# Kernel tuning notes

Hardware: AMD Instinct MI355X
Metric: run time of the kernel (lower is better)

## Reference

```python
import jax, jax.numpy as jnp
import numpy as np

# Per-task block sizes, sorted descending (powers of 2), as in _InverseLogDetCache
N = (262144, 65536, 16384)
TOTAL = 262144 + 65536 + 16384  # 344064
DIAG_SHIFT = 10.0  # keeps Schur complement S away from 0 (plays role of noise)


def setup_inputs() -> dict:
    key = jax.random.key(0)
    ks = jax.random.split(key, 14)
    rn = lambda k, n: jax.random.normal(k, (n,), dtype=jnp.float32)
    return {
        "lam00_re": rn(ks[0], N[0]) + DIAG_SHIFT,
        "lam00_im": rn(ks[1], N[0]),
        "lam01_re": rn(ks[2], N[0]),
        "lam01_im": rn(ks[3], N[0]),
        "lam02_re": rn(ks[4], N[0]),
        "lam02_im": rn(ks[5], N[0]),
        "lam11_re": rn(ks[6], N[1]) + DIAG_SHIFT,
        "lam11_im": rn(ks[7], N[1]),
        "lam12_re": rn(ks[8], N[1]),
        "lam12_im": rn(ks[9], N[1]),
        "lam22_re": rn(ks[10], N[2]) + DIAG_SHIFT,
        "lam22_im": rn(ks[11], N[2]),
        "z_re": rn(ks[12], TOTAL),
        "z_im": rn(ks[13], TOTAL),
    }


def _step(A, B, lam_ll, n_l):
    """One recursive block Schur-complement update.
    A: (Ra, Ra, na) complex current inverse; B: (Ra*r, n_l) off-diag lam block;
    lam_ll: (n_l,) diagonal lam; returns updated A (R+1, R+1, n_l) and logdet inc."""
    Ra, na = A.shape[0], A.shape[-1]
    r = na // n_l
    Bvec = B.reshape(Ra, -1)                              # (Ra, na)
    T = (Bvec[None, :, :] * A).sum(1).reshape(-1, n_l)    # (R, n_l), R = Ra*r
    M = (B.conj() * T).sum(0)                             # (n_l,)
    S = lam_ll - M                                        # Schur complement diag
    logdet_inc = jnp.log(jnp.abs(S)).sum()
    P = T / S                                             # (R, n_l)
    C = P[:, None, :] * T[None, :, :].conj()              # (R, R, n_l)
    # scatter-add old inverse A into the refined block structure of C
    ii0, ii1, ii2 = jnp.meshgrid(jnp.arange(Ra), jnp.arange(Ra), jnp.arange(na), indexing='ij')
    ii0, ii1, ii2 = ii0.ravel(), ii1.ravel(), ii2.ravel()
    jj0 = ii2 % n_l
    jj1 = ii2 // n_l
    C = C.at[ii0 * r + jj1, ii1 * r + jj1, jj0].add(A.reshape(-1))
    ur = jnp.concatenate([C, -P[:, None, :]], axis=1)                       # (R, R+1, n_l)
    br = jnp.concatenate([-P.conj()[None, :, :], (1.0 / S)[None, None, :]], axis=1)  # (1, R+1, n_l)
    return jnp.concatenate([ur, br], axis=0), logdet_inc


def _forward(lams, z):
    A = (1.0 / lams[(0, 0)])[None, None, :]               # (1, 1, N[0])
    logdet = jnp.log(jnp.abs(lams[(0, 0)])).sum()
    for l in range(1, len(N)):
        B = jnp.concatenate([lams[(k, l)] for k in range(l)], axis=0).reshape(-1, N[l])
        A, inc = _step(A, B, lams[(l, l)], N[l])
        logdet = logdet + inc
    # tilde-to-tilde gram matrix solve: z (TOTAL,) -> (1, R, n_min) * A, sum block rows
    n_min = N[-1]
    zb = z.reshape(1, -1, n_min)                          # (1, 21, n_min)
    zout = (zb * A).sum(-2).reshape(-1)                   # (TOTAL,)
    return A, logdet, zout


def reference(lam00_re, lam00_im, lam01_re, lam01_im, lam02_re, lam02_im,
              lam11_re, lam11_im, lam12_re, lam12_im, lam22_re, lam22_im,
              z_re, z_im):
    lams = {
        (0, 0): lam00_re + 1j * lam00_im,
        (0, 1): lam01_re + 1j * lam01_im,
        (0, 2): lam02_re + 1j * lam02_im,
        (1, 1): lam11_re + 1j * lam11_im,
        (1, 2): lam12_re + 1j * lam12_im,
        (2, 2): lam22_re + 1j * lam22_im,
    }
    z = z_re + 1j * z_im
    A, logdet, zout = _forward(lams, z)
    return (jnp.stack([A.real, A.imag]), logdet, jnp.stack([zout.real, zout.imag]))
```

## Files before the change

### kernel.cpp

```cpp
#include <hip/hip_runtime.h>

#define N2 16384
#define N1 65536

#define OUT_AIM 7225344
#define OUT_LD  14450688
#define OUT_ZRE 14450689
#define OUT_ZIM 14794753

#define L_T2R  0
#define L_T2I  1280
#define L_M2   2560
#define L_SC   3072
#define L_IS2R 9728
#define L_IS2I 9792
#define L_RED  9856
#define L_TOT  9864

#define SC(idx, u, jl) lds[L_SC + (((idx)*4 + (u)) * 64) + (jl)]

__global__ __launch_bounds__(448) void fused_kernel(
    const float* __restrict__ l00r, const float* __restrict__ l00i,
    const float* __restrict__ l01r, const float* __restrict__ l01i,
    const float* __restrict__ l02r, const float* __restrict__ l02i,
    const float* __restrict__ l11r, const float* __restrict__ l11i,
    const float* __restrict__ l12r, const float* __restrict__ l12i,
    const float* __restrict__ l22r, const float* __restrict__ l22i,
    const float* __restrict__ zre,  const float* __restrict__ zim,
    float* __restrict__ out, double* __restrict__ ld_partial)
{
    __shared__ float lds[L_TOT];
    const int t   = threadIdx.x;
    const int jl  = t & 63;
    const int j0  = blockIdx.x * 64;
    const bool y0 = (blockIdx.y == 0);
    float ld = 0.f;

    if (t < 256) {
        const int u = t >> 6;
        const int m = u * N2 + (j0 + jl);

        float i0r[4], i0i[4], t1r[4], t1i[4], p1r[4], p1i[4];
        float m1r = 0.f, m1i = 0.f;
#pragma unroll
        for (int k = 0; k < 4; ++k) {
            const int i = k * N1 + m;
            const float ar = l00r[i], ai = l00i[i];
            const float br = l01r[i], bi = l01i[i];
            const float d  = ar*ar + ai*ai;
            const float rd = 1.f / d;
            if (y0) ld += 0.5f * logf(d);
            const float xr = ar * rd, xi = -ai * rd;
            i0r[k] = xr; i0i[k] = xi;
            const float tr = br*xr - bi*xi;
            const float ti = br*xi + bi*xr;
            t1r[k] = tr; t1i[k] = ti;
            m1r += br*tr + bi*ti;
            m1i += br*ti - bi*tr;
        }
        const float s1r = l11r[m] - m1r;
        const float s1i = l11i[m] - m1i;
        const float ds1 = s1r*s1r + s1i*s1i;
        if (y0) ld += 0.5f * logf(ds1);
        const float rds1 = 1.f / ds1;
        const float is1r = s1r * rds1, is1i = -s1i * rds1;
#pragma unroll
        for (int k = 0; k < 4; ++k) {
            p1r[k] = t1r[k]*is1r - t1i[k]*is1i;
            p1i[k] = t1r[k]*is1i + t1i[k]*is1r;
        }

        float bcr[5], bci[5];
#pragma unroll
        for (int a = 0; a < 4; ++a) { bcr[a] = l02r[a*N1+m]; bci[a] = l02i[a*N1+m]; }
        bcr[4] = l12r[m]; bci[4] = l12i[m];

        float wr = -bcr[4], wi = -bci[4];
#pragma unroll
        for (int b = 0; b < 4; ++b) {
            wr += bcr[b]*t1r[b] + bci[b]*t1i[b];
            wi += bci[b]*t1r[b] - bcr[b]*t1i[b];
        }
        float ur[5], ui[5];
#pragma unroll
        for (int a = 0; a < 4; ++a) {
            ur[a] = p1r[a]*wr - p1i[a]*wi + bcr[a]*i0r[a] - bci[a]*i0i[a];
            ui[a] = p1r[a]*wi + p1i[a]*wr + bcr[a]*i0i[a] + bci[a]*i0r[a];
        }
        {
            float vr = bcr[4]*is1r - bci[4]*is1i;
            float vi = bcr[4]*is1i + bci[4]*is1r;
#pragma unroll
            for (int b = 0; b < 4; ++b) {
                vr -= bcr[b]*p1r[b] + bci[b]*p1i[b];
                vi -= bci[b]*p1r[b] - bcr[b]*p1i[b];
            }
            ur[4] = vr; ui[4] = vi;
        }
        float m2r = 0.f, m2i = 0.f;
#pragma unroll
        for (int a = 0; a < 5; ++a) {
            lds[L_T2R + (a*4+u)*64 + jl] = ur[a];
            lds[L_T2I + (a*4+u)*64 + jl] = ui[a];
            m2r += bcr[a]*ur[a] + bci[a]*ui[a];
            m2i += bcr[a]*ui[a] - bci[a]*ur[a];
        }
        lds[L_M2 + (0*4+u)*64 + jl] = m2r;
        lds[L_M2 + (1*4+u)*64 + jl] = m2i;
#pragma unroll
        for (int b = 0; b < 4; ++b) {
            SC(b,      u, jl) = t1r[b];  SC(4+b,  u, jl) = t1i[b];
            SC(8+b,    u, jl) = p1r[b];  SC(12+b, u, jl) = p1i[b];
            SC(16+b,   u, jl) = i0r[b];  SC(20+b, u, jl) = i0i[b];
        }
        SC(24, u, jl) = is1r;  SC(25, u, jl) = is1i;
    }
    __syncthreads();

    if (t < 64) {
        float s2r = l22r[j0 + t], s2i = l22i[j0 + t];
#pragma unroll
        for (int u = 0; u < 4; ++u) {
            s2r -= lds[L_M2 + (0*4+u)*64 + t];
            s2i -= lds[L_M2 + (1*4+u)*64 + t];
        }
        const float ds2  = s2r*s2r + s2i*s2i;
        const float rds2 = 1.f / ds2;
        lds[L_IS2R + t] =  s2r * rds2;
        lds[L_IS2I + t] = -s2i * rds2;
        if (y0) ld += 0.5f * logf(ds2);
    }
    __syncthreads();

    const int g = t >> 6;
    const int p = blockIdx.y * 7 + g;
    const int j = j0 + jl;
    const float is2r = lds[L_IS2R + jl];
    const float is2i = lds[L_IS2I + jl];

    float zr[21], zi[21];
#pragma unroll
    for (int q = 0; q < 21; ++q) { zr[q] = zre[q*N2+j]; zi[q] = zim[q*N2+j]; }

    float zar = 0.f, zai = 0.f;
    if (p == 20) {
#pragma unroll
        for (int q = 0; q < 21; ++q) {
            float ar, ai;
            if (q < 20) {
                const float tqr = lds[L_T2R + q*64 + jl];
                const float tqi = lds[L_T2I + q*64 + jl];
                ar = -(tqr*is2r - tqi*is2i);
                ai =  (tqr*is2i + tqi*is2r);
            } else { ar = is2r; ai = is2i; }
            out[(p*21 + q)*N2 + j]           = ar;
            out[OUT_AIM + (p*21 + q)*N2 + j] = ai;
            zar += zr[q]*ar - zi[q]*ai;
            zai += zr[q]*ai + zi[q]*ar;
        }
    } else {
        const int a_p = p >> 2, u_p = p & 3;
        const float tpr = lds[L_T2R + p*64 + jl];
        const float tpi = lds[L_T2I + p*64 + jl];
        const float ppr = tpr*is2r - tpi*is2i;
        const float ppi = tpr*is2i + tpi*is2r;
        float sar[5], sai[5];
        if (a_p < 4) {
            const float par = SC(8+a_p, u_p, jl), pai = SC(12+a_p, u_p, jl);
#pragma unroll
            for (int b = 0; b < 4; ++b) {
                const float tbr = SC(b, u_p, jl), tbi = SC(4+b, u_p, jl);
                sar[b] = par*tbr + pai*tbi;
                sai[b] = pai*tbr - par*tbi;
            }
            sar[a_p] += SC(16+a_p, u_p, jl);
            sai[a_p] += SC(20+a_p, u_p, jl);
            sar[4] = -par; sai[4] = -pai;
        } else {
#pragma unroll
            for (int b = 0; b < 4; ++b) {
                sar[b] = -SC(8+b,  u_p, jl);
                sai[b] =  SC(12+b, u_p, jl);
            }
            sar[4] = SC(24, u_p, jl);
            sai[4] = SC(25, u_p, jl);
        }
#pragma unroll
        for (int q = 0; q < 21; ++q) {
            float ar, ai;
            if (q < 20) {
                const float tqr = lds[L_T2R + q*64 + jl];
                const float tqi = lds[L_T2I + q*64 + jl];
                ar = ppr*tqr + ppi*tqi;
                ai = ppi*tqr - ppr*tqi;
                if ((q & 3) == u_p) { ar += sar[q>>2]; ai += sai[q>>2]; }
            } else { ar = -ppr; ai = -ppi; }
            out[(p*21 + q)*N2 + j]           = ar;
            out[OUT_AIM + (p*21 + q)*N2 + j] = ai;
            zar += zr[q]*ar - zi[q]*ai;
            zai += zr[q]*ai + zi[q]*ar;
        }
    }
    out[OUT_ZRE + p*N2 + j] = zar;
    out[OUT_ZIM + p*N2 + j] = zai;

    if (y0) {
        float v = ld;
#pragma unroll
        for (int off = 32; off > 0; off >>= 1) v += __shfl_down(v, off, 64);
        __syncthreads();
        if (jl == 0) lds[L_RED + g] = v;
        __syncthreads();
        if (t == 0) {
            double s = 0.0;
#pragma unroll
            for (int w = 0; w < 7; ++w) s += (double)lds[L_RED + w];
            ld_partial[blockIdx.x] = s;
        }
    }
}

__global__ void finalize_kernel(const double* __restrict__ part,
                                float* __restrict__ out) {
    double v = part[threadIdx.x];
#pragma unroll
    for (int off = 32; off > 0; off >>= 1) v += __shfl_down(v, off, 64);
    __shared__ double wsum[4];
    if ((threadIdx.x & 63) == 0) wsum[threadIdx.x >> 6] = v;
    __syncthreads();
    if (threadIdx.x == 0)
        out[OUT_LD] = (float)(wsum[0] + wsum[1] + wsum[2] + wsum[3]);
}

extern "C" void kernel_launch(void* const* d_in, const int* in_sizes, int n_in,
                              void* d_out, int out_size, void* d_ws, size_t ws_size,
                              hipStream_t stream)
{
    const float* l00r = (const float*)d_in[0];
    const float* l00i = (const float*)d_in[1];
    const float* l01r = (const float*)d_in[2];
    const float* l01i = (const float*)d_in[3];
    const float* l02r = (const float*)d_in[4];
    const float* l02i = (const float*)d_in[5];
    const float* l11r = (const float*)d_in[6];
    const float* l11i = (const float*)d_in[7];
    const float* l12r = (const float*)d_in[8];
    const float* l12i = (const float*)d_in[9];
    const float* l22r = (const float*)d_in[10];
    const float* l22i = (const float*)d_in[11];
    const float* zre  = (const float*)d_in[12];
    const float* zim  = (const float*)d_in[13];
    float*  out        = (float*)d_out;
    double* ld_partial = (double*)d_ws;

    fused_kernel<<<dim3(N2/64, 3), dim3(448), 0, stream>>>(
        l00r,l00i,l01r,l01i,l02r,l02i,l11r,l11i,l12r,l12i,l22r,l22i,
        zre,zim, out, ld_partial);
    finalize_kernel<<<1, 256, 0, stream>>>(ld_partial, out);
}
```

Before: 111.7 us.

## Split output rows across 6 y-blocks of 256 threads with trimmed shared memory

Changes the grid from 3 y-blocks of 448 threads to 6 y-blocks of 256 threads, so every thread joins the Schur-complement prologue and each wave produces one output row. Each block now stores in LDS only the per-row scalars its rows need, which shrinks shared memory and raises occupancy through launch_bounds(256,4). Output stores become nontemporal, and z is loaded inside the loop rather than kept in 42 registers. The cost is that the prologue (l00/l01/l11 loads and the first-step math) is recomputed in 6 blocks instead of 3, and the last y-block runs only one useful wave.

Result: slower. 114.8 us (+2.8%).

```diff
diff --git a/kernel.cpp b/kernel.cpp
--- a/kernel.cpp
+++ b/kernel.cpp
@@ -12,14 +12,14 @@
 #define L_T2I  1280
 #define L_M2   2560
 #define L_SC   3072
-#define L_IS2R 9728
-#define L_IS2I 9792
-#define L_RED  9856
-#define L_TOT  9864
-
-#define SC(idx, u, jl) lds[L_SC + (((idx)*4 + (u)) * 64) + (jl)]
-
-__global__ __launch_bounds__(448) void fused_kernel(
+#define L_IS2R 6144
+#define L_IS2I 6208
+#define L_RED  6272
+#define L_TOT  6276
+
+#define SC(idx, uu, jj) lds[L_SC + (((idx)*4 + (uu)) * 64) + (jj)]
+
+__global__ __launch_bounds__(256, 4) void fused_kernel(
     const float* __restrict__ l00r, const float* __restrict__ l00i,
     const float* __restrict__ l01r, const float* __restrict__ l01i,
     const float* __restrict__ l02r, const float* __restrict__ l02i,
@@ -32,12 +32,13 @@
     __shared__ float lds[L_TOT];
     const int t   = threadIdx.x;
     const int jl  = t & 63;
+    const int u   = t >> 6;
     const int j0  = blockIdx.x * 64;
-    const bool y0 = (blockIdx.y == 0);
+    const int y   = blockIdx.y;
+    const bool y0 = (y == 0);
     float ld = 0.f;
 
-    if (t < 256) {
-        const int u = t >> 6;
+    {
         const int m = u * N2 + (j0 + jl);
 
         float i0r[4], i0i[4], t1r[4], t1i[4], p1r[4], p1i[4];
@@ -107,22 +108,30 @@
         }
         lds[L_M2 + (0*4+u)*64 + jl] = m2r;
         lds[L_M2 + (1*4+u)*64 + jl] = m2i;
-#pragma unroll
-        for (int b = 0; b < 4; ++b) {
-            SC(b,      u, jl) = t1r[b];  SC(4+b,  u, jl) = t1i[b];
-            SC(8+b,    u, jl) = p1r[b];  SC(12+b, u, jl) = p1i[b];
-            SC(16+b,   u, jl) = i0r[b];  SC(20+b, u, jl) = i0i[b];
-        }
-        SC(24, u, jl) = is1r;  SC(25, u, jl) = is1i;
+
+        if (y < 4) {
+#pragma unroll
+            for (int b = 0; b < 4; ++b) {
+                SC(b,   u, jl) = t1r[b];  SC(4+b, u, jl) = t1i[b];
+            }
+            SC(8,  u, jl) = p1r[y];  SC(9,  u, jl) = p1i[y];
+            SC(10, u, jl) = i0r[y];  SC(11, u, jl) = i0i[y];
+        } else if (y == 4) {
+#pragma unroll
+            for (int b = 0; b < 4; ++b) {
+                SC(b,   u, jl) = p1r[b];  SC(4+b, u, jl) = p1i[b];
+            }
+            SC(8, u, jl) = is1r;  SC(9, u, jl) = is1i;
+        }
     }
     __syncthreads();
 
     if (t < 64) {
         float s2r = l22r[j0 + t], s2i = l22i[j0 + t];
 #pragma unroll
-        for (int u = 0; u < 4; ++u) {
-            s2r -= lds[L_M2 + (0*4+u)*64 + t];
-            s2i -= lds[L_M2 + (1*4+u)*64 + t];
+        for (int uu = 0; uu < 4; ++uu) {
+            s2r -= lds[L_M2 + (0*4+uu)*64 + t];
+            s2i -= lds[L_M2 + (1*4+uu)*64 + t];
         }
         const float ds2  = s2r*s2r + s2i*s2i;
         const float rds2 = 1.f / ds2;
@@ -132,89 +141,88 @@
     }
     __syncthreads();
 
-    const int g = t >> 6;
-    const int p = blockIdx.y * 7 + g;
+    const int g = u;
+    const int p = y * 4 + g;
     const int j = j0 + jl;
-    const float is2r = lds[L_IS2R + jl];
-    const float is2i = lds[L_IS2I + jl];
-
-    float zr[21], zi[21];
-#pragma unroll
-    for (int q = 0; q < 21; ++q) { zr[q] = zre[q*N2+j]; zi[q] = zim[q*N2+j]; }
-
-    float zar = 0.f, zai = 0.f;
-    if (p == 20) {
-#pragma unroll
-        for (int q = 0; q < 21; ++q) {
-            float ar, ai;
-            if (q < 20) {
-                const float tqr = lds[L_T2R + q*64 + jl];
-                const float tqi = lds[L_T2I + q*64 + jl];
-                ar = -(tqr*is2r - tqi*is2i);
-                ai =  (tqr*is2i + tqi*is2r);
-            } else { ar = is2r; ai = is2i; }
-            out[(p*21 + q)*N2 + j]           = ar;
-            out[OUT_AIM + (p*21 + q)*N2 + j] = ai;
-            zar += zr[q]*ar - zi[q]*ai;
-            zai += zr[q]*ai + zi[q]*ar;
-        }
-    } else {
-        const int a_p = p >> 2, u_p = p & 3;
-        const float tpr = lds[L_T2R + p*64 + jl];
-        const float tpi = lds[L_T2I + p*64 + jl];
-        const float ppr = tpr*is2r - tpi*is2i;
-        const float ppi = tpr*is2i + tpi*is2r;
-        float sar[5], sai[5];
-        if (a_p < 4) {
-            const float par = SC(8+a_p, u_p, jl), pai = SC(12+a_p, u_p, jl);
-#pragma unroll
-            for (int b = 0; b < 4; ++b) {
-                const float tbr = SC(b, u_p, jl), tbi = SC(4+b, u_p, jl);
-                sar[b] = par*tbr + pai*tbi;
-                sai[b] = pai*tbr - par*tbi;
-            }
-            sar[a_p] += SC(16+a_p, u_p, jl);
-            sai[a_p] += SC(20+a_p, u_p, jl);
-            sar[4] = -par; sai[4] = -pai;
+
+    if (p <= 20) {
+        const float is2r = lds[L_IS2R + jl];
+        const float is2i = lds[L_IS2I + jl];
+        float zar = 0.f, zai = 0.f;
+
+        if (p == 20) {
+#pragma unroll
+            for (int q = 0; q < 21; ++q) {
+                float ar, ai;
+                if (q < 20) {
+                    const float tqr = lds[L_T2R + q*64 + jl];
+                    const float tqi = lds[L_T2I + q*64 + jl];
+                    ar = -(tqr*is2r - tqi*is2i);
+                    ai =  (tqr*is2i + tqi*is2r);
+                } else { ar = is2r; ai = is2i; }
+                __builtin_nontemporal_store(ar, out + (p*21+q)*N2 + j);
+                __builtin_nontemporal_store(ai, out + OUT_AIM + (p*21+q)*N2 + j);
+                const float zqr = zre[q*N2+j], zqi = zim[q*N2+j];
+                zar += zqr*ar - zqi*ai;
+                zai += zqr*ai + zqi*ar;
+            }
         } else {
-#pragma unroll
-            for (int b = 0; b < 4; ++b) {
-                sar[b] = -SC(8+b,  u_p, jl);
-                sai[b] =  SC(12+b, u_p, jl);
-            }
-            sar[4] = SC(24, u_p, jl);
-            sai[4] = SC(25, u_p, jl);
-        }
-#pragma unroll
-        for (int q = 0; q < 21; ++q) {
-            float ar, ai;
-            if (q < 20) {
-                const float tqr = lds[L_T2R + q*64 + jl];
-                const float tqi = lds[L_T2I + q*64 + jl];
-                ar = ppr*tqr + ppi*tqi;
-                ai = ppi*tqr - ppr*tqi;
-                if ((q & 3) == u_p) { ar += sar[q>>2]; ai += sai[q>>2]; }
-            } else { ar = -ppr; ai = -ppi; }
-            out[(p*21 + q)*N2 + j]           = ar;
-            out[OUT_AIM + (p*21 + q)*N2 + j] = ai;
-            zar += zr[q]*ar - zi[q]*ai;
-            zai += zr[q]*ai + zi[q]*ar;
-        }
-    }
-    out[OUT_ZRE + p*N2 + j] = zar;
-    out[OUT_ZIM + p*N2 + j] = zai;
+            const float tpr = lds[L_T2R + p*64 + jl];
+            const float tpi = lds[L_T2I + p*64 + jl];
+            const float ppr = tpr*is2r - tpi*is2i;
+            const float ppi = tpr*is2i + tpi*is2r;
+            float sar[5], sai[5];
+            if (y < 4) {
+                const float par = SC(8, g, jl), pai = SC(9, g, jl);
+#pragma unroll
+                for (int b = 0; b < 4; ++b) {
+                    const float tbr = SC(b, g, jl), tbi = SC(4+b, g, jl);
+                    sar[b] = par*tbr + pai*tbi;
+                    sai[b] = pai*tbr - par*tbi;
+                }
+                sar[y] += SC(10, g, jl);
+                sai[y] += SC(11, g, jl);
+                sar[4] = -par; sai[4] = -pai;
+            } else {
+#pragma unroll
+                for (int b = 0; b < 4; ++b) {
+                    sar[b] = -SC(b,   g, jl);
+                    sai[b] =  SC(4+b, g, jl);
+                }
+                sar[4] = SC(8, g, jl);
+                sai[4] = SC(9, g, jl);
+            }
+#pragma unroll
+            for (int q = 0; q < 21; ++q) {
+                float ar, ai;
+                if (q < 20) {
+                    const float tqr = lds[L_T2R + q*64 + jl];
+                    const float tqi = lds[L_T2I + q*64 + jl];
+                    ar = ppr*tqr + ppi*tqi;
+                    ai = ppi*tqr - ppr*tqi;
+                    if ((q & 3) == g) { ar += sar[q>>2]; ai += sai[q>>2]; }
+                } else { ar = -ppr; ai = -ppi; }
+                __builtin_nontemporal_store(ar, out + (p*21+q)*N2 + j);
+                __builtin_nontemporal_store(ai, out + OUT_AIM + (p*21+q)*N2 + j);
+                const float zqr = zre[q*N2+j], zqi = zim[q*N2+j];
+                zar += zqr*ar - zqi*ai;
+                zai += zqr*ai + zqi*ar;
+            }
+        }
+        __builtin_nontemporal_store(zar, out + OUT_ZRE + p*N2 + j);
+        __builtin_nontemporal_store(zai, out + OUT_ZIM + p*N2 + j);
+    }
 
     if (y0) {
         float v = ld;
 #pragma unroll
         for (int off = 32; off > 0; off >>= 1) v += __shfl_down(v, off, 64);
-        __syncthreads();
         if (jl == 0) lds[L_RED + g] = v;
         __syncthreads();
         if (t == 0) {
             double s = 0.0;
 #pragma unroll
-            for (int w = 0; w < 7; ++w) s += (double)lds[L_RED + w];
+            for (int w = 0; w < 4; ++w) s += (double)lds[L_RED + w];
             ld_partial[blockIdx.x] = s;
         }
     }
@@ -253,7 +261,7 @@
     float*  out        = (float*)d_out;
     double* ld_partial = (double*)d_ws;
 
-    fused_kernel<<<dim3(N2/64, 3), dim3(448), 0, stream>>>(
+    fused_kernel<<<dim3(N2/64, 6), dim3(256), 0, stream>>>(
         l00r,l00i,l01r,l01i,l02r,l02i,l11r,l11i,l12r,l12i,l22r,l22i,
         zre,zim, out, ld_partial);
     finalize_kernel<<<1, 256, 0, stream>>>(ld_partial, out);
```

## Remap output phase to float4 columns per lane with nontemporal vector stores

Applied to the files above, without the earlier changes.

The final output phase is remapped so each lane owns four contiguous columns and a quarter of the 21 q-rows, instead of one column and all 21 rows. The A matrix and the z inputs then move as 128-bit vector loads and nontemporal vector stores. The z-output partial sums are combined across the four lane groups with cross-lane shuffles. A minimum-occupancy hint is added to the launch bounds. The goal is to cut store instruction count and improve write coalescing on this write-heavy kernel, at the cost of more index logic, extra shuffles, and possible register pressure from the occupancy hint.

Measured after the change: 113.4 us. About the same (+1.6%).

```diff
diff --git a/kernel.cpp b/kernel.cpp
--- a/kernel.cpp
+++ b/kernel.cpp
@@ -2,6 +2,8 @@
 
 #define N2 16384
 #define N1 65536
+
+typedef float vf4 __attribute__((ext_vector_type(4)));
 
 #define OUT_AIM 7225344
 #define OUT_LD  14450688
@@ -19,7 +21,7 @@
 
 #define SC(idx, u, jl) lds[L_SC + (((idx)*4 + (u)) * 64) + (jl)]
 
-__global__ __launch_bounds__(448) void fused_kernel(
+__global__ __launch_bounds__(448, 4) void fused_kernel(
     const float* __restrict__ l00r, const float* __restrict__ l00i,
     const float* __restrict__ l01r, const float* __restrict__ l01i,
     const float* __restrict__ l02r, const float* __restrict__ l02i,
@@ -120,9 +122,9 @@
     if (t < 64) {
         float s2r = l22r[j0 + t], s2i = l22i[j0 + t];
 #pragma unroll
-        for (int u = 0; u < 4; ++u) {
-            s2r -= lds[L_M2 + (0*4+u)*64 + t];
-            s2i -= lds[L_M2 + (1*4+u)*64 + t];
+        for (int uu = 0; uu < 4; ++uu) {
+            s2r -= lds[L_M2 + (0*4+uu)*64 + t];
+            s2i -= lds[L_M2 + (1*4+uu)*64 + t];
         }
         const float ds2  = s2r*s2r + s2i*s2i;
         const float rds2 = 1.f / ds2;
@@ -132,77 +134,114 @@
     }
     __syncthreads();
 
-    const int g = t >> 6;
-    const int p = blockIdx.y * 7 + g;
-    const int j = j0 + jl;
-    const float is2r = lds[L_IS2R + jl];
-    const float is2i = lds[L_IS2I + jl];
-
-    float zr[21], zi[21];
-#pragma unroll
-    for (int q = 0; q < 21; ++q) { zr[q] = zre[q*N2+j]; zi[q] = zim[q*N2+j]; }
-
-    float zar = 0.f, zai = 0.f;
-    if (p == 20) {
-#pragma unroll
-        for (int q = 0; q < 21; ++q) {
-            float ar, ai;
+    const int g  = t >> 6;
+    const int p  = blockIdx.y * 7 + g;
+    const int l  = t & 63;
+    const int h  = l >> 4;
+    const int c4 = (l & 15) * 4;
+    const int j4 = j0 + c4;
+
+    const vf4 is2r = *(const vf4*)&lds[L_IS2R + c4];
+    const vf4 is2i = *(const vf4*)&lds[L_IS2I + c4];
+
+    float zar[4] = {0,0,0,0}, zai[4] = {0,0,0,0};
+
+    float ppr[4], ppi[4];
+    float sar[4], sai[4];
+    const int a_p = p >> 2, u_p = p & 3;
+    if (p < 20) {
+        const vf4 tpr = *(const vf4*)&lds[L_T2R + p*64 + c4];
+        const vf4 tpi = *(const vf4*)&lds[L_T2I + p*64 + c4];
+#pragma unroll
+        for (int e = 0; e < 4; ++e) {
+            ppr[e] = tpr[e]*is2r[e] - tpi[e]*is2i[e];
+            ppi[e] = tpr[e]*is2i[e] + tpi[e]*is2r[e];
+        }
+    }
+
+#pragma unroll
+    for (int qi = 0; qi < 6; ++qi) {
+        const int q = 4*qi + h;
+        if (q > 20) continue;
+        vf4 ar4, ai4;
+        const bool do_sc = (p < 20) && (h == u_p) && (qi < 5);
+        if (do_sc) {
+            if (a_p < 4) {
+#pragma unroll
+                for (int e = 0; e < 4; ++e) {
+                    const int jc = c4 + e;
+                    const float par = SC(8+a_p, u_p, jc), pai = SC(12+a_p, u_p, jc);
+                    if (qi < 4) {
+                        const float tbr = SC(qi, u_p, jc), tbi = SC(4+qi, u_p, jc);
+                        float vr = par*tbr + pai*tbi;
+                        float vi = pai*tbr - par*tbi;
+                        if (qi == a_p) { vr += SC(16+a_p, u_p, jc); vi += SC(20+a_p, u_p, jc); }
+                        sar[e] = vr; sai[e] = vi;
+                    } else { sar[e] = -par; sai[e] = -pai; }
+                }
+            } else {
+#pragma unroll
+                for (int e = 0; e < 4; ++e) {
+                    const int jc = c4 + e;
+                    if (qi < 4) { sar[e] = -SC(8+qi, u_p, jc); sai[e] = SC(12+qi, u_p, jc); }
+                    else        { sar[e] =  SC(24,   u_p, jc); sai[e] = SC(25,   u_p, jc); }
+                }
+            }
+        }
+        if (p == 20) {
             if (q < 20) {
-                const float tqr = lds[L_T2R + q*64 + jl];
-                const float tqi = lds[L_T2I + q*64 + jl];
-                ar = -(tqr*is2r - tqi*is2i);
-                ai =  (tqr*is2i + tqi*is2r);
-            } else { ar = is2r; ai = is2i; }
-            out[(p*21 + q)*N2 + j]           = ar;
-            out[OUT_AIM + (p*21 + q)*N2 + j] = ai;
-            zar += zr[q]*ar - zi[q]*ai;
-            zai += zr[q]*ai + zi[q]*ar;
-        }
-    } else {
-        const int a_p = p >> 2, u_p = p & 3;
-        const float tpr = lds[L_T2R + p*64 + jl];
-        const float tpi = lds[L_T2I + p*64 + jl];
-        const float ppr = tpr*is2r - tpi*is2i;
-        const float ppi = tpr*is2i + tpi*is2r;
-        float sar[5], sai[5];
-        if (a_p < 4) {
-            const float par = SC(8+a_p, u_p, jl), pai = SC(12+a_p, u_p, jl);
-#pragma unroll
-            for (int b = 0; b < 4; ++b) {
-                const float tbr = SC(b, u_p, jl), tbi = SC(4+b, u_p, jl);
-                sar[b] = par*tbr + pai*tbi;
-                sai[b] = pai*tbr - par*tbi;
+                const vf4 tr = *(const vf4*)&lds[L_T2R + q*64 + c4];
+                const vf4 ti = *(const vf4*)&lds[L_T2I + q*64 + c4];
+#pragma unroll
+                for (int e = 0; e < 4; ++e) {
+                    ar4[e] = -(tr[e]*is2r[e] - ti[e]*is2i[e]);
+                    ai4[e] =  (tr[e]*is2i[e] + ti[e]*is2r[e]);
+                }
+            } else { ar4 = is2r; ai4 = is2i; }
+        } else {
+            if (q < 20) {
+                const vf4 tr = *(const vf4*)&lds[L_T2R + q*64 + c4];
+                const vf4 ti = *(const vf4*)&lds[L_T2I + q*64 + c4];
+#pragma unroll
+                for (int e = 0; e < 4; ++e) {
+                    float vr = ppr[e]*tr[e] + ppi[e]*ti[e];
+                    float vi = ppi[e]*tr[e] - ppr[e]*ti[e];
+                    if (do_sc) { vr += sar[e]; vi += sai[e]; }
+                    ar4[e] = vr; ai4[e] = vi;
+                }
+            } else {
+#pragma unroll
+                for (int e = 0; e < 4; ++e) { ar4[e] = -ppr[e]; ai4[e] = -ppi[e]; }
             }
-            sar[a_p] += SC(16+a_p, u_p, jl);
-            sai[a_p] += SC(20+a_p, u_p, jl);
-            sar[4] = -par; sai[4] = -pai;
-        } else {
-#pragma unroll
-            for (int b = 0; b < 4; ++b) {
-                sar[b] = -SC(8+b,  u_p, jl);
-                sai[b] =  SC(12+b, u_p, jl);
-            }
-            sar[4] = SC(24, u_p, jl);
-            sai[4] = SC(25, u_p, jl);
-        }
-#pragma unroll
-        for (int q = 0; q < 21; ++q) {
-            float ar, ai;
-            if (q < 20) {
-                const float tqr = lds[L_T2R + q*64 + jl];
-                const float tqi = lds[L_T2I + q*64 + jl];
-                ar = ppr*tqr + ppi*tqi;
-                ai = ppi*tqr - ppr*tqi;
-                if ((q & 3) == u_p) { ar += sar[q>>2]; ai += sai[q>>2]; }
-            } else { ar = -ppr; ai = -ppi; }
-            out[(p*21 + q)*N2 + j]           = ar;
-            out[OUT_AIM + (p*21 + q)*N2 + j] = ai;
-            zar += zr[q]*ar - zi[q]*ai;
-            zai += zr[q]*ai + zi[q]*ar;
-        }
-    }
-    out[OUT_ZRE + p*N2 + j] = zar;
-    out[OUT_ZIM + p*N2 + j] = zai;
+        }
+        __builtin_nontemporal_store(ar4, (vf4*)(out + (p*21+q)*N2 + j4));
+        __builtin_nontemporal_store(ai4, (vf4*)(out + OUT_AIM + (p*21+q)*N2 + j4));
+        const vf4 zr4 = *(const vf4*)(zre + q*N2 + j4);
+        const vf4 zi4 = *(const vf4*)(zim + q*N2 + j4);
+#pragma unroll
+        for (int e = 0; e < 4; ++e) {
+            zar[e] += zr4[e]*ar4[e] - zi4[e]*ai4[e];
+            zai[e] += zr4[e]*ai4[e] + zi4[e]*ar4[e];
+        }
+    }
+
+#pragma unroll
+    for (int e = 0; e < 4; ++e) {
+        zar[e] += __shfl_xor(zar[e], 16, 64);  zar[e] += __shfl_xor(zar[e], 32, 64);
+        zai[e] += __shfl_xor(zai[e], 16, 64);  zai[e] += __shfl_xor(zai[e], 32, 64);
+    }
+    {
+        const int src = l >> 2;
+        const float r0 = __shfl(zar[0], src, 64), r1 = __shfl(zar[1], src, 64);
+        const float r2 = __shfl(zar[2], src, 64), r3 = __shfl(zar[3], src, 64);
+        const float i0 = __shfl(zai[0], src, 64), i1 = __shfl(zai[1], src, 64);
+        const float i2 = __shfl(zai[2], src, 64), i3 = __shfl(zai[3], src, 64);
+        const int e = l & 3;
+        const float zvr = e==0 ? r0 : e==1 ? r1 : e==2 ? r2 : r3;
+        const float zvi = e==0 ? i0 : e==1 ? i1 : e==2 ? i2 : i3;
+        __builtin_nontemporal_store(zvr, out + OUT_ZRE + p*N2 + j0 + l);
+        __builtin_nontemporal_store(zvi, out + OUT_ZIM + p*N2 + j0 + l);
+    }
 
     if (y0) {
         float v = ld;
```
